# Optimization experiments

Measured on AMD Instinct MI355X. Metric: run time of the kernel, lower is better.

## Reference

```python
import jax, jax.numpy as jnp
import numpy as np

N, E, IN, C, F = 100000, 3200000, 128, 4, 16


def setup_inputs() -> dict:
    key = jax.random.key(0)
    ks = jax.random.split(key, 8)
    return {
        "node_feat": jax.random.normal(ks[0], (N, IN), dtype=jnp.float32),
        "edge_feat": jax.random.normal(ks[1], (E, C), dtype=jnp.float32),
        "src": jax.random.randint(ks[2], (E,), 0, N, dtype=jnp.int32),
        "dst": jax.random.randint(ks[3], (E,), 0, N, dtype=jnp.int32),
        "Wfc": jax.random.normal(ks[4], (C * F, IN), dtype=jnp.float32) * 0.05,
        "We": jax.random.normal(ks[5], (C, C), dtype=jnp.float32) * 0.3,
        "attn_l": jax.random.normal(ks[6], (1, C, F), dtype=jnp.float32) * 0.1,
        "attn_r": jax.random.normal(ks[7], (1, C, F), dtype=jnp.float32) * 0.1,
    }


def reference(node_feat, edge_feat, src, dst, Wfc, We, attn_l, attn_r):
    n = node_feat.shape[0]
    # fc(h).view(-1, C, F)  (shared src/dst projection)
    feat = (node_feat @ Wfc.T).reshape(n, C, F)            # [N, C, F]
    # edge_fc(edge_feat).view(-1, C, 1)
    e_feat = edge_feat @ We.T                               # [E, C]
    # el/er: (feat * attn).sum(-1)
    el = jnp.sum(feat * attn_l, axis=-1)                    # [N, C]
    er = jnp.sum(feat * attn_r, axis=-1)                    # [N, C]
    # u_add_v -> leaky_relu -> * edge feature
    e = jax.nn.leaky_relu(el[src] + er[dst], negative_slope=0.2) * e_feat  # [E, C]
    # edge_softmax grouped by destination node (numerically stable)
    m = jax.ops.segment_max(e, dst, num_segments=n)         # [N, C]
    ee = jnp.exp(e - m[dst])                                # [E, C]
    s = jax.ops.segment_sum(ee, dst, num_segments=n)        # [N, C]
    a = ee / s[dst]                                         # [E, C]
    # message passing: sum_e a_e * ft_src(e)  (standard EGAT aggregation)
    msg = feat[src] * a[:, :, None]                         # [E, C, F]
    rst = jax.ops.segment_sum(msg, dst, num_segments=n)     # [N, C, F]
    return rst
```

## Files before the change

kernel.cpp:

```cpp
#include <hip/hip_runtime.h>
#include <hip/hip_fp16.h>

#define N_NODES 100000
#define N_EDGES 3200000
#define E0 1601536
#define E1REM 1598464
#define BUCKET_NODES 128
#define NB 782
#define NBC 25
#define CNODES 4096
#define CHA 4096
#define NPA0 391
#define NPA1 391
#define CHB 4096
#define NPB0 391
#define NPB1 391
#define FS_CAP 4608
#define NPROJ 782
#define NG64 1563
#define NHIST 512

typedef __attribute__((ext_vector_type(8))) short bf16x8;
typedef __attribute__((ext_vector_type(4))) float f32x4;

__device__ __forceinline__ unsigned short f2bf(float f) {
    unsigned u = __float_as_uint(f);
    unsigned r = (u + 0x7FFFu + ((u >> 16) & 1u)) >> 16;
    return (unsigned short)r;
}
__device__ __forceinline__ float bf2f(unsigned short h) {
    return __uint_as_float(((unsigned)h) << 16);
}

__global__ __launch_bounds__(256) void node_proj(
    const float* __restrict__ node_feat,
    const float* __restrict__ Wfc,
    const float* __restrict__ attn_l,
    const float* __restrict__ attn_r,
    unsigned short* __restrict__ featb,
    float* __restrict__ el,
    float* __restrict__ er)
{
    __shared__ short Wb[8192];
    const int tid = threadIdx.x;
    for (int i = tid; i < 8192; i += 256) {
        const int e   = i & 7;
        const int col = (i >> 3) & 15;
        const int q   = (i >> 7) & 3;
        const int kk  = (i >> 9) & 3;
        const int t   = (i >> 11) & 3;
        Wb[i] = (short)f2bf(Wfc[(t * 16 + col) * 128 + kk * 32 + q * 8 + e]);
    }
    __syncthreads();

    const int lane = tid & 63;
    const int w = tid >> 6;
    const int col = lane & 15;
    const int q = lane >> 4;

    float alv[4], arv[4];
    #pragma unroll
    for (int t = 0; t < 4; ++t) {
        alv[t] = attn_l[t * 16 + col];
        arv[t] = attn_r[t * 16 + col];
    }

    for (int g = blockIdx.x; g < NG64; g += NPROJ) {
        const int n0 = g * 64 + w * 16;
        if (n0 >= N_NODES) continue;

        f32x4 acc0 = {0.f,0.f,0.f,0.f}, acc1 = {0.f,0.f,0.f,0.f};
        f32x4 acc2 = {0.f,0.f,0.f,0.f}, acc3 = {0.f,0.f,0.f,0.f};

        #pragma unroll
        for (int kk = 0; kk < 4; ++kk) {
            const float* ap = node_feat + (size_t)(n0 + col) * 128 + kk * 32 + q * 8;
            const float4 a0 = *(const float4*)ap;
            const float4 a1 = *(const float4*)(ap + 4);
            bf16x8 af;
            af[0] = (short)f2bf(a0.x); af[1] = (short)f2bf(a0.y);
            af[2] = (short)f2bf(a0.z); af[3] = (short)f2bf(a0.w);
            af[4] = (short)f2bf(a1.x); af[5] = (short)f2bf(a1.y);
            af[6] = (short)f2bf(a1.z); af[7] = (short)f2bf(a1.w);

            const bf16x8 b0 = *(const bf16x8*)&Wb[(((0*4+kk)*4+q)*16 + col)*8];
            const bf16x8 b1 = *(const bf16x8*)&Wb[(((1*4+kk)*4+q)*16 + col)*8];
            const bf16x8 b2 = *(const bf16x8*)&Wb[(((2*4+kk)*4+q)*16 + col)*8];
            const bf16x8 b3 = *(const bf16x8*)&Wb[(((3*4+kk)*4+q)*16 + col)*8];
            acc0 = __builtin_amdgcn_mfma_f32_16x16x32_bf16(af, b0, acc0, 0, 0, 0);
            acc1 = __builtin_amdgcn_mfma_f32_16x16x32_bf16(af, b1, acc1, 0, 0, 0);
            acc2 = __builtin_amdgcn_mfma_f32_16x16x32_bf16(af, b2, acc2, 0, 0, 0);
            acc3 = __builtin_amdgcn_mfma_f32_16x16x32_bf16(af, b3, acc3, 0, 0, 0);
        }

        #pragma unroll
        for (int m = 0; m < 4; ++m) {
            const size_t rb = (size_t)(n0 + q * 4 + m) * 64;
            featb[rb + 0 * 16 + col] = f2bf(acc0[m]);
            featb[rb + 1 * 16 + col] = f2bf(acc1[m]);
            featb[rb + 2 * 16 + col] = f2bf(acc2[m]);
            featb[rb + 3 * 16 + col] = f2bf(acc3[m]);
        }

        #pragma unroll
        for (int m = 0; m < 4; ++m) {
            float pl0 = acc0[m] * alv[0], pr0 = acc0[m] * arv[0];
            float pl1 = acc1[m] * alv[1], pr1 = acc1[m] * arv[1];
            float pl2 = acc2[m] * alv[2], pr2 = acc2[m] * arv[2];
            float pl3 = acc3[m] * alv[3], pr3 = acc3[m] * arv[3];
            #pragma unroll
            for (int off = 8; off >= 1; off >>= 1) {
                pl0 += __shfl_xor(pl0, off); pr0 += __shfl_xor(pr0, off);
                pl1 += __shfl_xor(pl1, off); pr1 += __shfl_xor(pr1, off);
                pl2 += __shfl_xor(pl2, off); pr2 += __shfl_xor(pr2, off);
                pl3 += __shfl_xor(pl3, off); pr3 += __shfl_xor(pr3, off);
            }
            if (col == 0) {
                const size_t eb = (size_t)(n0 + q * 4 + m) * 4;
                el[eb + 0] = pl0; el[eb + 1] = pl1; el[eb + 2] = pl2; el[eb + 3] = pl3;
                er[eb + 0] = pr0; er[eb + 1] = pr1; er[eb + 2] = pr2; er[eb + 3] = pr3;
            }
        }
    }
}

__global__ __launch_bounds__(256) void fhist(
    const int* __restrict__ dst,
    int* __restrict__ hhtot)
{
    __shared__ int h[2 * NB];
    const int tid = threadIdx.x;
    for (int i = tid; i < 2 * NB; i += 256) h[i] = 0;
    __syncthreads();
    const int stride = NHIST * 256;
    const int n4 = N_EDGES / 4;
    for (int idx = blockIdx.x * 256 + tid; idx < n4; idx += stride) {
        const int4 d4 = ((const int4*)dst)[idx];
        const int off = (idx * 4 >= E0) ? NB : 0;
        atomicAdd(&h[off + (d4.x >> 7)], 1);
        atomicAdd(&h[off + (d4.y >> 7)], 1);
        atomicAdd(&h[off + (d4.z >> 7)], 1);
        atomicAdd(&h[off + (d4.w >> 7)], 1);
    }
    __syncthreads();
    for (int i = tid; i < 2 * NB; i += 256)
        if (h[i]) atomicAdd(&hhtot[i], h[i]);
}

__global__ __launch_bounds__(64) void bscan(const int* __restrict__ hhtot,
                                            int* __restrict__ base,
                                            int* __restrict__ fcursor,
                                            int* __restrict__ cbaseH,
                                            int* __restrict__ ccursorH)
{
    const int lane = threadIdx.x;
    int carry = 0;
    for (int ch = 0; ch < NB; ch += 64) {
        const int idx = ch + lane;
        const int v = (idx < NB) ? (hhtot[idx] + hhtot[NB + idx]) : 0;
        int x = v;
        #pragma unroll
        for (int off = 1; off < 64; off <<= 1) {
            int y = __shfl_up(x, off);
            if (lane >= off) x += y;
        }
        const int excl = x - v + carry;
        if (idx < NB) { base[idx] = excl; fcursor[idx] = excl; }
        carry += __shfl(x, 63);
    }
    if (lane == 0) base[NB] = carry;

    for (int h2 = 0; h2 < 2; ++h2) {
        int v = 0;
        if (lane < NBC) {
            const int f0 = lane * 32;
            const int f1 = min(f0 + 32, NB);
            for (int f = f0; f < f1; ++f) v += hhtot[h2 * NB + f];
        }
        int x = v;
        #pragma unroll
        for (int off = 1; off < 64; off <<= 1) {
            int y = __shfl_up(x, off);
            if (lane >= off) x += y;
        }
        const int excl = x - v;
        if (lane <= NBC) cbaseH[h2 * (NBC + 1) + lane] = excl;
        if (lane < NBC) ccursorH[h2 * NBC + lane] = excl;
    }
}

__device__ __forceinline__ void passA_body(
    unsigned char* smem,
    const int* __restrict__ src,
    const int* __restrict__ dst,
    const float* __restrict__ edge_feat,
    const float* __restrict__ We,
    const float* __restrict__ el,
    const float* __restrict__ er,
    int* __restrict__ ccursorH,
    uint3* __restrict__ wA,
    int half, int blk)
{
    int* ldst  = (int*)smem;
    int* lbase = (int*)(smem + 16384);
    int* lcnt  = (int*)(smem + 16512);
    const int tid = threadIdx.x;
    if (tid < NBC) lcnt[tid] = 0;
    __syncthreads();
    const int hbeg = half ? E0 : 0;
    const int hend = half ? N_EDGES : E0;
    const int e0 = hbeg + blk * CHA;
    const int n = min(CHA, hend - e0);
    for (int i = tid; i < n; i += 1024) {
        const int d = dst[e0 + i];
        ldst[i] = d;
        atomicAdd(&lcnt[d >> 12], 1);
    }
    __syncthreads();
    if (tid < NBC) {
        const int c = lcnt[tid];
        lbase[tid] = c ? atomicAdd(&ccursorH[half * NBC + tid], c) : 0;
        lcnt[tid] = 0;
    }
    __syncthreads();

    const float4 W0 = ((const float4*)We)[0];
    const float4 W1 = ((const float4*)We)[1];
    const float4 W2 = ((const float4*)We)[2];
    const float4 W3 = ((const float4*)We)[3];

    for (int i = tid; i < n; i += 1024) {
        const int e = e0 + i;
        const int d = ldst[i];
        const int cb = d >> 12;
        const int r = atomicAdd(&lcnt[cb], 1);
        const int pos = lbase[cb] + r;

        const int s = src[e];
        const float4 ef = ((const float4*)edge_feat)[e];
        const float4 l4 = ((const float4*)el)[s];
        const float4 r4 = ((const float4*)er)[d];

        float t0 = l4.x + r4.x; t0 = t0 > 0.f ? t0 : 0.2f * t0;
        float t1 = l4.y + r4.y; t1 = t1 > 0.f ? t1 : 0.2f * t1;
        float t2 = l4.z + r4.z; t2 = t2 > 0.f ? t2 : 0.2f * t2;
        float t3 = l4.w + r4.w; t3 = t3 > 0.f ? t3 : 0.2f * t3;

        const float ee0 = __expf(t0 * (W0.x * ef.x + W0.y * ef.y + W0.z * ef.z + W0.w * ef.w));
        const float ee1 = __expf(t1 * (W1.x * ef.x + W1.y * ef.y + W1.z * ef.z + W1.w * ef.w));
        const float ee2 = __expf(t2 * (W2.x * ef.x + W2.y * ef.y + W2.z * ef.z + W2.w * ef.w));
        const float ee3 = __expf(t3 * (W3.x * ef.x + W3.y * ef.y + W3.z * ef.z + W3.w * ef.w));

        const unsigned h0 = __half_as_ushort(__float2half_rn(ee0));
        const unsigned h1 = __half_as_ushort(__float2half_rn(ee1));
        const unsigned h2 = __half_as_ushort(__float2half_rn(ee2));
        const unsigned h3 = __half_as_ushort(__float2half_rn(ee3));

        wA[pos] = make_uint3((unsigned)s | ((unsigned)(d & (CNODES - 1)) << 17),
                             h0 | (h1 << 16), h2 | (h3 << 16));
    }
}

__device__ __forceinline__ void passB_body(
    unsigned char* smem,
    const int* __restrict__ cbaseH,
    int* __restrict__ fcursor,
    const uint3* __restrict__ wA,
    uint3* __restrict__ wB,
    int half, int blk)
{
    int* lcb   = (int*)smem;
    int* lbase = (int*)(smem + 112);
    int* lcnt  = (int*)(smem + 3240);
    unsigned short* sfid = (unsigned short*)(smem + 6368);
    uint3* sx  = (uint3*)(smem + 14576);
    const int tid = threadIdx.x;
    for (int i = tid; i < NB; i += 1024) lcnt[i] = 0;
    if (tid < NBC + 1) lcb[tid] = cbaseH[half * (NBC + 1) + tid];
    __syncthreads();

    const int hsz = half ? E1REM : E0;
    const int p0 = blk * CHB;
    const int n = min(CHB, hsz - p0);
    for (int i = tid; i < n; i += 1024) {
        const uint3 x = wA[p0 + i];
        sx[i] = x;
        const int pos = p0 + i;
        int lo = 0, hi = NBC;
        while (lo + 1 < hi) {
            const int mid = (lo + hi) >> 1;
            if (lcb[mid] <= pos) lo = mid; else hi = mid;
        }
        const int dst12 = (int)((x.x >> 17) & (CNODES - 1));
        const int fid = lo * 32 + (dst12 >> 7);
        sfid[i] = (unsigned short)fid;
        atomicAdd(&lcnt[fid], 1);
    }
    __syncthreads();
    for (int b = tid; b < NB; b += 1024) {
        const int c = lcnt[b];
        lbase[b] = c ? atomicAdd(&fcursor[b], c) : 0;
        lcnt[b] = 0;
    }
    __syncthreads();
    for (int i = tid; i < n; i += 1024) {
        const uint3 x = sx[i];
        const int fid = sfid[i];
        const int r = atomicAdd(&lcnt[fid], 1);
        const unsigned dl = (x.x >> 17) & (BUCKET_NODES - 1);
        wB[lbase[fid] + r] = make_uint3((x.x & 0x1FFFFu) | (dl << 17), x.y, x.z);
    }
}

__global__ __launch_bounds__(1024) void passA(
    const int* __restrict__ src, const int* __restrict__ dst,
    const float* __restrict__ edge_feat, const float* __restrict__ We,
    const float* __restrict__ el, const float* __restrict__ er,
    int* __restrict__ ccursorH, uint3* __restrict__ wA, int half)
{
    __shared__ __align__(16) unsigned char smem[16640];
    passA_body(smem, src, dst, edge_feat, We, el, er, ccursorH, wA, half, blockIdx.x);
}

__global__ __launch_bounds__(1024) void passB(
    const int* __restrict__ cbaseH, int* __restrict__ fcursor,
    const uint3* __restrict__ wA, uint3* __restrict__ wB, int half)
{
    __shared__ __align__(16) unsigned char smem[63728];
    passB_body(smem, cbaseH, fcursor, wA, wB, half, blockIdx.x);
}

__global__ __launch_bounds__(1024) void finesort(
    const int* __restrict__ base,
    uint3* __restrict__ wP,
    int* __restrict__ node_off)
{
    __shared__ uint3 sP[FS_CAP];
    __shared__ int hist[BUCKET_NODES];
    __shared__ int cur[BUCKET_NODES];
    const int b = blockIdx.x;
    const int s = base[b];
    int cnt = base[b + 1] - s;
    if (cnt > FS_CAP) cnt = FS_CAP;
    const int tid = threadIdx.x;
    if (tid < BUCKET_NODES) hist[tid] = 0;
    __syncthreads();
    for (int i = tid; i < cnt; i += 1024) {
        const uint3 p = wP[s + i];
        sP[i] = p;
        atomicAdd(&hist[(p.x >> 17) & (BUCKET_NODES - 1)], 1);
    }
    __syncthreads();
    if (tid < 64) {
        int carry = 0;
        for (int ch = 0; ch < BUCKET_NODES; ch += 64) {
            const int v = hist[ch + tid];
            int x = v;
            #pragma unroll
            for (int off = 1; off < 64; off <<= 1) {
                int y = __shfl_up(x, off);
                if (tid >= off) x += y;
            }
            const int excl = x - v + carry;
            cur[ch + tid] = excl;
            const int node = b * BUCKET_NODES + ch + tid;
            if (node < N_NODES) node_off[node] = s + excl;
            carry += __shfl(x, 63);
        }
        if (tid == 0 && b == NB - 1) node_off[N_NODES] = N_EDGES;
    }
    __syncthreads();
    for (int i = tid; i < cnt; i += 1024) {
        const uint3 p = sP[i];
        const int dl = (p.x >> 17) & (BUCKET_NODES - 1);
        const int r = atomicAdd(&cur[dl], 1);
        wP[s + r] = make_uint3((p.x & 0x1FFFFu) << 7, p.y, p.z);
    }
}

__global__ __launch_bounds__(256) void aggregate(
    const int* __restrict__ node_off,
    const uint3* __restrict__ wP,
    const unsigned short* __restrict__ featb,
    float* __restrict__ rst)
{
    __shared__ float lee[4][64][4];
    __shared__ unsigned lsi[4][64];
    const int tid = threadIdx.x;
    const int node = (int)((blockIdx.x * 256 + tid) >> 6);
    const int lane = tid & 63;
    const int w = tid >> 6;
    if (node >= N_NODES) return;
    const int half = lane >> 5;
    const int j = lane & 31;
    const int cc = j >> 3;
    const unsigned jByte = (unsigned)j * 4u;
    const unsigned char* __restrict__ fbyte = (const unsigned char*)featb;

    const int start = node_off[node];
    const int end = node_off[node + 1];

    float acc0 = 0.f, acc1 = 0.f;
    float s0 = 0.f, s1 = 0.f, s2 = 0.f, s3 = 0.f;

    for (int bat = start; bat < end; bat += 64) {
        const int n = min(64, end - bat);
        if (lane < n) {
            const uint3 p = wP[bat + lane];
            const float e0 = __half2float(__ushort_as_half((unsigned short)(p.y & 0xffffu)));
            const float e1 = __half2float(__ushort_as_half((unsigned short)(p.y >> 16)));
            const float e2 = __half2float(__ushort_as_half((unsigned short)(p.z & 0xffffu)));
            const float e3 = __half2float(__ushort_as_half((unsigned short)(p.z >> 16)));
            lsi[w][lane] = p.x;
            *(float4*)&lee[w][lane][0] = make_float4(e0, e1, e2, e3);
            s0 += e0; s1 += e1; s2 += e2; s3 += e3;
        } else {
            lsi[w][lane] = 0;
            *(float4*)&lee[w][lane][0] = make_float4(0.f, 0.f, 0.f, 0.f);
        }
        __builtin_amdgcn_wave_barrier();
        const int iters = (n + 1) >> 1;
        for (int i = 0; i < iters; ++i) {
            const int e = 2 * i + half;
            const unsigned so = lsi[w][e];
            const float eec = lee[w][e][cc];
            const unsigned fr = *(const unsigned*)(fbyte + so + jByte);
            acc0 = fmaf(eec, bf2f((unsigned short)(fr & 0xffffu)), acc0);
            acc1 = fmaf(eec, bf2f((unsigned short)(fr >> 16)), acc1);
        }
        __builtin_amdgcn_wave_barrier();
    }

    acc0 += __shfl_xor(acc0, 32);
    acc1 += __shfl_xor(acc1, 32);

    #pragma unroll
    for (int off = 32; off >= 1; off >>= 1) {
        s0 += __shfl_xor(s0, off);
        s1 += __shfl_xor(s1, off);
        s2 += __shfl_xor(s2, off);
        s3 += __shfl_xor(s3, off);
    }

    const float v0 = __shfl(acc0, lane >> 1);
    const float v1 = __shfl(acc1, lane >> 1);
    const float accL = (lane & 1) ? v1 : v0;
    const int c = lane >> 4;
    const float ssum = (c == 0) ? s0 : ((c == 1) ? s1 : ((c == 2) ? s2 : s3));
    rst[(size_t)node * 64 + lane] = (end > start) ? accL / ssum : 0.f;
}

extern "C" void kernel_launch(void* const* d_in, const int* in_sizes, int n_in,
                              void* d_out, int out_size, void* d_ws, size_t ws_size,
                              hipStream_t stream)
{
    const float* node_feat = (const float*)d_in[0];
    const float* edge_feat = (const float*)d_in[1];
    const int*   src       = (const int*)d_in[2];
    const int*   dst       = (const int*)d_in[3];
    const float* Wfc       = (const float*)d_in[4];
    const float* We        = (const float*)d_in[5];
    const float* attn_l    = (const float*)d_in[6];
    const float* attn_r    = (const float*)d_in[7];
    float* rst = (float*)d_out;

    char* ws = (char*)d_ws;
    unsigned short* featb = (unsigned short*)(ws);
    float* el       = (float*)(ws + 12800000);
    float* er       = (float*)(ws + 14400000);
    int*   hhtot    = (int*)  (ws + 16000000);
    int*   base     = (int*)  (ws + 16006400);
    int*   fcursor  = (int*)  (ws + 16009600);
    int*   cbaseH   = (int*)  (ws + 16012800);
    int*   ccursorH = (int*)  (ws + 16013056);
    int*   node_off = (int*)  (ws + 16013312);
    uint3* wB       = (uint3*)(ws + 16413952);
    uint3* wA = (uint3*)d_out;

    hipMemsetAsync(hhtot, 0, 2 * NB * sizeof(int), stream);

    node_proj<<<NPROJ, 256, 0, stream>>>(node_feat, Wfc, attn_l, attn_r, featb, el, er);
    fhist<<<NHIST, 256, 0, stream>>>(dst, hhtot);
    bscan<<<1, 64, 0, stream>>>(hhtot, base, fcursor, cbaseH, ccursorH);

    passA<<<NPA0, 1024, 0, stream>>>(src, dst, edge_feat, We, el, er, ccursorH, wA, 0);
    passB<<<NPB0, 1024, 0, stream>>>(cbaseH, fcursor, wA, wB, 0);
    passA<<<NPA1, 1024, 0, stream>>>(src, dst, edge_feat, We, el, er, ccursorH, wA, 1);
    passB<<<NPB1, 1024, 0, stream>>>(cbaseH, fcursor, wA, wB, 1);

    finesort<<<NB, 1024, 0, stream>>>(base, wB, node_off);
    aggregate<<<(N_NODES * 64 + 255) / 256, 256, 0, stream>>>(node_off, wB, featb, rst);
}
```

Baseline: 240.4 us.

## Replace two-level coarse/fine edge partition with single-pass scatter into fine buckets

```diff
diff --git a/kernel.cpp b/kernel.cpp
--- a/kernel.cpp
+++ b/kernel.cpp
@@ -3,18 +3,10 @@
 
 #define N_NODES 100000
 #define N_EDGES 3200000
-#define E0 1601536
-#define E1REM 1598464
 #define BUCKET_NODES 128
 #define NB 782
-#define NBC 25
-#define CNODES 4096
-#define CHA 4096
-#define NPA0 391
-#define NPA1 391
-#define CHB 4096
-#define NPB0 391
-#define NPB1 391
+#define CHS 8192
+#define NSC 391
 #define FS_CAP 4608
 #define NPROJ 782
 #define NG64 1563
@@ -126,38 +118,35 @@
 
 __global__ __launch_bounds__(256) void fhist(
     const int* __restrict__ dst,
-    int* __restrict__ hhtot)
-{
-    __shared__ int h[2 * NB];
-    const int tid = threadIdx.x;
-    for (int i = tid; i < 2 * NB; i += 256) h[i] = 0;
+    int* __restrict__ ftot)
+{
+    __shared__ int h[NB];
+    const int tid = threadIdx.x;
+    for (int i = tid; i < NB; i += 256) h[i] = 0;
     __syncthreads();
     const int stride = NHIST * 256;
     const int n4 = N_EDGES / 4;
     for (int idx = blockIdx.x * 256 + tid; idx < n4; idx += stride) {
         const int4 d4 = ((const int4*)dst)[idx];
-        const int off = (idx * 4 >= E0) ? NB : 0;
-        atomicAdd(&h[off + (d4.x >> 7)], 1);
-        atomicAdd(&h[off + (d4.y >> 7)], 1);
-        atomicAdd(&h[off + (d4.z >> 7)], 1);
-        atomicAdd(&h[off + (d4.w >> 7)], 1);
-    }
-    __syncthreads();
-    for (int i = tid; i < 2 * NB; i += 256)
-        if (h[i]) atomicAdd(&hhtot[i], h[i]);
-}
-
-__global__ __launch_bounds__(64) void bscan(const int* __restrict__ hhtot,
+        atomicAdd(&h[d4.x >> 7], 1);
+        atomicAdd(&h[d4.y >> 7], 1);
+        atomicAdd(&h[d4.z >> 7], 1);
+        atomicAdd(&h[d4.w >> 7], 1);
+    }
+    __syncthreads();
+    for (int i = tid; i < NB; i += 256)
+        if (h[i]) atomicAdd(&ftot[i], h[i]);
+}
+
+__global__ __launch_bounds__(64) void bscan(const int* __restrict__ ftot,
                                             int* __restrict__ base,
-                                            int* __restrict__ fcursor,
-                                            int* __restrict__ cbaseH,
-                                            int* __restrict__ ccursorH)
+                                            int* __restrict__ fcursor)
 {
     const int lane = threadIdx.x;
     int carry = 0;
     for (int ch = 0; ch < NB; ch += 64) {
         const int idx = ch + lane;
-        const int v = (idx < NB) ? (hhtot[idx] + hhtot[NB + idx]) : 0;
+        const int v = (idx < NB) ? ftot[idx] : 0;
         int x = v;
         #pragma unroll
         for (int off = 1; off < 64; off <<= 1) {
@@ -169,58 +158,36 @@
         carry += __shfl(x, 63);
     }
     if (lane == 0) base[NB] = carry;
-
-    for (int h2 = 0; h2 < 2; ++h2) {
-        int v = 0;
-        if (lane < NBC) {
-            const int f0 = lane * 32;
-            const int f1 = min(f0 + 32, NB);
-            for (int f = f0; f < f1; ++f) v += hhtot[h2 * NB + f];
-        }
-        int x = v;
-        #pragma unroll
-        for (int off = 1; off < 64; off <<= 1) {
-            int y = __shfl_up(x, off);
-            if (lane >= off) x += y;
-        }
-        const int excl = x - v;
-        if (lane <= NBC) cbaseH[h2 * (NBC + 1) + lane] = excl;
-        if (lane < NBC) ccursorH[h2 * NBC + lane] = excl;
-    }
-}
-
-__device__ __forceinline__ void passA_body(
-    unsigned char* smem,
+}
+
+__global__ __launch_bounds__(1024) void scatter(
     const int* __restrict__ src,
     const int* __restrict__ dst,
     const float* __restrict__ edge_feat,
     const float* __restrict__ We,
     const float* __restrict__ el,
     const float* __restrict__ er,
-    int* __restrict__ ccursorH,
-    uint3* __restrict__ wA,
-    int half, int blk)
-{
-    int* ldst  = (int*)smem;
-    int* lbase = (int*)(smem + 16384);
-    int* lcnt  = (int*)(smem + 16512);
-    const int tid = threadIdx.x;
-    if (tid < NBC) lcnt[tid] = 0;
-    __syncthreads();
-    const int hbeg = half ? E0 : 0;
-    const int hend = half ? N_EDGES : E0;
-    const int e0 = hbeg + blk * CHA;
-    const int n = min(CHA, hend - e0);
+    int* __restrict__ fcursor,
+    uint3* __restrict__ wB)
+{
+    __shared__ int ldst[CHS];
+    __shared__ int lbase[NB];
+    __shared__ int lcnt[NB];
+    const int tid = threadIdx.x;
+    for (int i = tid; i < NB; i += 1024) lcnt[i] = 0;
+    __syncthreads();
+    const int e0 = blockIdx.x * CHS;
+    const int n = min(CHS, N_EDGES - e0);
     for (int i = tid; i < n; i += 1024) {
         const int d = dst[e0 + i];
         ldst[i] = d;
-        atomicAdd(&lcnt[d >> 12], 1);
-    }
-    __syncthreads();
-    if (tid < NBC) {
-        const int c = lcnt[tid];
-        lbase[tid] = c ? atomicAdd(&ccursorH[half * NBC + tid], c) : 0;
-        lcnt[tid] = 0;
+        atomicAdd(&lcnt[d >> 7], 1);
+    }
+    __syncthreads();
+    for (int b = tid; b < NB; b += 1024) {
+        const int c = lcnt[b];
+        lbase[b] = c ? atomicAdd(&fcursor[b], c) : 0;
+        lcnt[b] = 0;
     }
     __syncthreads();
 
@@ -232,9 +199,9 @@
     for (int i = tid; i < n; i += 1024) {
         const int e = e0 + i;
         const int d = ldst[i];
-        const int cb = d >> 12;
-        const int r = atomicAdd(&lcnt[cb], 1);
-        const int pos = lbase[cb] + r;
+        const int fb = d >> 7;
+        const int r = atomicAdd(&lcnt[fb], 1);
+        const int pos = lbase[fb] + r;
 
         const int s = src[e];
         const float4 ef = ((const float4*)edge_feat)[e];
@@ -256,78 +223,9 @@
         const unsigned h2 = __half_as_ushort(__float2half_rn(ee2));
         const unsigned h3 = __half_as_ushort(__float2half_rn(ee3));
 
-        wA[pos] = make_uint3((unsigned)s | ((unsigned)(d & (CNODES - 1)) << 17),
+        wB[pos] = make_uint3((unsigned)s | ((unsigned)(d & (BUCKET_NODES - 1)) << 17),
                              h0 | (h1 << 16), h2 | (h3 << 16));
     }
-}
-
-__device__ __forceinline__ void passB_body(
-    unsigned char* smem,
-    const int* __restrict__ cbaseH,
-    int* __restrict__ fcursor,
-    const uint3* __restrict__ wA,
-    uint3* __restrict__ wB,
-    int half, int blk)
-{
-    int* lcb   = (int*)smem;
-    int* lbase = (int*)(smem + 112);
-    int* lcnt  = (int*)(smem + 3240);
-    unsigned short* sfid = (unsigned short*)(smem + 6368);
-    uint3* sx  = (uint3*)(smem + 14576);
-    const int tid = threadIdx.x;
-    for (int i = tid; i < NB; i += 1024) lcnt[i] = 0;
-    if (tid < NBC + 1) lcb[tid] = cbaseH[half * (NBC + 1) + tid];
-    __syncthreads();
-
-    const int hsz = half ? E1REM : E0;
-    const int p0 = blk * CHB;
-    const int n = min(CHB, hsz - p0);
-    for (int i = tid; i < n; i += 1024) {
-        const uint3 x = wA[p0 + i];
-        sx[i] = x;
-        const int pos = p0 + i;
-        int lo = 0, hi = NBC;
-        while (lo + 1 < hi) {
-            const int mid = (lo + hi) >> 1;
-            if (lcb[mid] <= pos) lo = mid; else hi = mid;
-        }
-        const int dst12 = (int)((x.x >> 17) & (CNODES - 1));
-        const int fid = lo * 32 + (dst12 >> 7);
-        sfid[i] = (unsigned short)fid;
-        atomicAdd(&lcnt[fid], 1);
-    }
-    __syncthreads();
-    for (int b = tid; b < NB; b += 1024) {
-        const int c = lcnt[b];
-        lbase[b] = c ? atomicAdd(&fcursor[b], c) : 0;
-        lcnt[b] = 0;
-    }
-    __syncthreads();
-    for (int i = tid; i < n; i += 1024) {
-        const uint3 x = sx[i];
-        const int fid = sfid[i];
-        const int r = atomicAdd(&lcnt[fid], 1);
-        const unsigned dl = (x.x >> 17) & (BUCKET_NODES - 1);
-        wB[lbase[fid] + r] = make_uint3((x.x & 0x1FFFFu) | (dl << 17), x.y, x.z);
-    }
-}
-
-__global__ __launch_bounds__(1024) void passA(
-    const int* __restrict__ src, const int* __restrict__ dst,
-    const float* __restrict__ edge_feat, const float* __restrict__ We,
-    const float* __restrict__ el, const float* __restrict__ er,
-    int* __restrict__ ccursorH, uint3* __restrict__ wA, int half)
-{
-    __shared__ __align__(16) unsigned char smem[16640];
-    passA_body(smem, src, dst, edge_feat, We, el, er, ccursorH, wA, half, blockIdx.x);
-}
-
-__global__ __launch_bounds__(1024) void passB(
-    const int* __restrict__ cbaseH, int* __restrict__ fcursor,
-    const uint3* __restrict__ wA, uint3* __restrict__ wB, int half)
-{
-    __shared__ __align__(16) unsigned char smem[63728];
-    passB_body(smem, cbaseH, fcursor, wA, wB, half, blockIdx.x);
 }
 
 __global__ __launch_bounds__(1024) void finesort(
@@ -468,26 +366,18 @@
     unsigned short* featb = (unsigned short*)(ws);
     float* el       = (float*)(ws + 12800000);
     float* er       = (float*)(ws + 14400000);
-    int*   hhtot    = (int*)  (ws + 16000000);
-    int*   base     = (int*)  (ws + 16006400);
-    int*   fcursor  = (int*)  (ws + 16009600);
-    int*   cbaseH   = (int*)  (ws + 16012800);
-    int*   ccursorH = (int*)  (ws + 16013056);
-    int*   node_off = (int*)  (ws + 16013312);
-    uint3* wB       = (uint3*)(ws + 16413952);
-    uint3* wA = (uint3*)d_out;
-
-    hipMemsetAsync(hhtot, 0, 2 * NB * sizeof(int), stream);
+    int*   ftot     = (int*)  (ws + 16000000);
+    int*   base     = (int*)  (ws + 16003200);
+    int*   fcursor  = (int*)  (ws + 16006400);
+    int*   node_off = (int*)  (ws + 16009600);
+    uint3* wB       = (uint3*)(ws + 16409728);
+
+    hipMemsetAsync(ftot, 0, NB * sizeof(int), stream);
 
     node_proj<<<NPROJ, 256, 0, stream>>>(node_feat, Wfc, attn_l, attn_r, featb, el, er);
-    fhist<<<NHIST, 256, 0, stream>>>(dst, hhtot);
-    bscan<<<1, 64, 0, stream>>>(hhtot, base, fcursor, cbaseH, ccursorH);
-
-    passA<<<NPA0, 1024, 0, stream>>>(src, dst, edge_feat, We, el, er, ccursorH, wA, 0);
-    passB<<<NPB0, 1024, 0, stream>>>(cbaseH, fcursor, wA, wB, 0);
-    passA<<<NPA1, 1024, 0, stream>>>(src, dst, edge_feat, We, el, er, ccursorH, wA, 1);
-    passB<<<NPB1, 1024, 0, stream>>>(cbaseH, fcursor, wA, wB, 1);
-
+    fhist<<<NHIST, 256, 0, stream>>>(dst, ftot);
+    bscan<<<1, 64, 0, stream>>>(ftot, base, fcursor);
+    scatter<<<NSC, 1024, 0, stream>>>(src, dst, edge_feat, We, el, er, fcursor, wB);
     finesort<<<NB, 1024, 0, stream>>>(base, wB, node_off);
     aggregate<<<(N_NODES * 64 + 255) / 256, 256, 0, stream>>>(node_off, wB, featb, rst);
 }
```

New measurement: 270.9 us. +12.7%, slower.

## Fuse per-bucket fine sort with aggregation using an LDS permutation index

Applied to the files above, without the earlier changes.

```diff
diff --git a/kernel.cpp b/kernel.cpp
--- a/kernel.cpp
+++ b/kernel.cpp
@@ -330,13 +330,17 @@
     passB_body(smem, cbaseH, fcursor, wA, wB, half, blockIdx.x);
 }
 
-__global__ __launch_bounds__(1024) void finesort(
+__global__ __launch_bounds__(1024) void sort_agg(
     const int* __restrict__ base,
-    uint3* __restrict__ wP,
-    int* __restrict__ node_off)
-{
-    __shared__ uint3 sP[FS_CAP];
+    const uint3* __restrict__ wP,
+    const unsigned short* __restrict__ featb,
+    float* __restrict__ rst)
+{
+    __shared__ unsigned sA[FS_CAP];
+    __shared__ unsigned sE[FS_CAP * 2];
+    __shared__ unsigned short inv[FS_CAP];
     __shared__ int hist[BUCKET_NODES];
+    __shared__ int off[BUCKET_NODES + 1];
     __shared__ int cur[BUCKET_NODES];
     const int b = blockIdx.x;
     const int s = base[b];
@@ -345,109 +349,89 @@
     const int tid = threadIdx.x;
     if (tid < BUCKET_NODES) hist[tid] = 0;
     __syncthreads();
+
     for (int i = tid; i < cnt; i += 1024) {
         const uint3 p = wP[s + i];
-        sP[i] = p;
+        sA[i] = p.x;
+        sE[2 * i]     = p.y;
+        sE[2 * i + 1] = p.z;
         atomicAdd(&hist[(p.x >> 17) & (BUCKET_NODES - 1)], 1);
     }
     __syncthreads();
+
     if (tid < 64) {
         int carry = 0;
         for (int ch = 0; ch < BUCKET_NODES; ch += 64) {
             const int v = hist[ch + tid];
             int x = v;
             #pragma unroll
-            for (int off = 1; off < 64; off <<= 1) {
-                int y = __shfl_up(x, off);
-                if (tid >= off) x += y;
+            for (int o = 1; o < 64; o <<= 1) {
+                int y = __shfl_up(x, o);
+                if (tid >= o) x += y;
             }
             const int excl = x - v + carry;
+            off[ch + tid] = excl;
             cur[ch + tid] = excl;
-            const int node = b * BUCKET_NODES + ch + tid;
-            if (node < N_NODES) node_off[node] = s + excl;
             carry += __shfl(x, 63);
         }
-        if (tid == 0 && b == NB - 1) node_off[N_NODES] = N_EDGES;
-    }
-    __syncthreads();
+        if (tid == 0) off[BUCKET_NODES] = carry;
+    }
+    __syncthreads();
+
     for (int i = tid; i < cnt; i += 1024) {
-        const uint3 p = sP[i];
-        const int dl = (p.x >> 17) & (BUCKET_NODES - 1);
+        const unsigned a = sA[i];
+        const int dl = (int)((a >> 17) & (BUCKET_NODES - 1));
         const int r = atomicAdd(&cur[dl], 1);
-        wP[s + r] = make_uint3((p.x & 0x1FFFFu) << 7, p.y, p.z);
-    }
-}
-
-__global__ __launch_bounds__(256) void aggregate(
-    const int* __restrict__ node_off,
-    const uint3* __restrict__ wP,
-    const unsigned short* __restrict__ featb,
-    float* __restrict__ rst)
-{
-    __shared__ float lee[4][64][4];
-    __shared__ unsigned lsi[4][64];
-    const int tid = threadIdx.x;
-    const int node = (int)((blockIdx.x * 256 + tid) >> 6);
+        inv[r] = (unsigned short)i;
+        sA[i] = (a & 0x1FFFFu) << 7;
+    }
+    __syncthreads();
+
     const int lane = tid & 63;
     const int w = tid >> 6;
-    if (node >= N_NODES) return;
     const int half = lane >> 5;
     const int j = lane & 31;
     const int cc = j >> 3;
     const unsigned jByte = (unsigned)j * 4u;
     const unsigned char* __restrict__ fbyte = (const unsigned char*)featb;
-
-    const int start = node_off[node];
-    const int end = node_off[node + 1];
-
-    float acc0 = 0.f, acc1 = 0.f;
-    float s0 = 0.f, s1 = 0.f, s2 = 0.f, s3 = 0.f;
-
-    for (int bat = start; bat < end; bat += 64) {
-        const int n = min(64, end - bat);
-        if (lane < n) {
-            const uint3 p = wP[bat + lane];
-            const float e0 = __half2float(__ushort_as_half((unsigned short)(p.y & 0xffffu)));
-            const float e1 = __half2float(__ushort_as_half((unsigned short)(p.y >> 16)));
-            const float e2 = __half2float(__ushort_as_half((unsigned short)(p.z & 0xffffu)));
-            const float e3 = __half2float(__ushort_as_half((unsigned short)(p.z >> 16)));
-            lsi[w][lane] = p.x;
-            *(float4*)&lee[w][lane][0] = make_float4(e0, e1, e2, e3);
-            s0 += e0; s1 += e1; s2 += e2; s3 += e3;
-        } else {
-            lsi[w][lane] = 0;
-            *(float4*)&lee[w][lane][0] = make_float4(0.f, 0.f, 0.f, 0.f);
-        }
-        __builtin_amdgcn_wave_barrier();
-        const int iters = (n + 1) >> 1;
+    const int node0 = b * BUCKET_NODES;
+
+    #pragma unroll 1
+    for (int nn = 0; nn < 8; ++nn) {
+        const int nl = w * 8 + nn;
+        const int node = node0 + nl;
+        if (node >= N_NODES) break;
+        const int st = off[nl];
+        const int deg = off[nl + 1] - st;
+
+        float acc0 = 0.f, acc1 = 0.f, scc = 0.f;
+        const int iters = (deg + 1) >> 1;
         for (int i = 0; i < iters; ++i) {
-            const int e = 2 * i + half;
-            const unsigned so = lsi[w][e];
-            const float eec = lee[w][e][cc];
+            const int o = 2 * i + half;
+            const bool valid = o < deg;
+            const int pos = valid ? (st + o) : 0;
+            const int idx = (int)inv[pos];
+            const unsigned so = sA[idx];
+            const unsigned ed = sE[2 * idx + (cc >> 1)];
+            float eec = __half2float(__ushort_as_half(
+                (unsigned short)((cc & 1) ? (ed >> 16) : (ed & 0xffffu))));
+            if (!valid) eec = 0.f;
             const unsigned fr = *(const unsigned*)(fbyte + so + jByte);
             acc0 = fmaf(eec, bf2f((unsigned short)(fr & 0xffffu)), acc0);
             acc1 = fmaf(eec, bf2f((unsigned short)(fr >> 16)), acc1);
-        }
-        __builtin_amdgcn_wave_barrier();
-    }
-
-    acc0 += __shfl_xor(acc0, 32);
-    acc1 += __shfl_xor(acc1, 32);
-
-    #pragma unroll
-    for (int off = 32; off >= 1; off >>= 1) {
-        s0 += __shfl_xor(s0, off);
-        s1 += __shfl_xor(s1, off);
-        s2 += __shfl_xor(s2, off);
-        s3 += __shfl_xor(s3, off);
-    }
-
-    const float v0 = __shfl(acc0, lane >> 1);
-    const float v1 = __shfl(acc1, lane >> 1);
-    const float accL = (lane & 1) ? v1 : v0;
-    const int c = lane >> 4;
-    const float ssum = (c == 0) ? s0 : ((c == 1) ? s1 : ((c == 2) ? s2 : s3));
-    rst[(size_t)node * 64 + lane] = (end > start) ? accL / ssum : 0.f;
+            scc += eec;
+        }
+
+        const float a0 = acc0 + __shfl_xor(acc0, 32);
+        const float a1 = acc1 + __shfl_xor(acc1, 32);
+        const float ss = scc + __shfl_xor(scc, 32);
+
+        const float v0 = __shfl(a0, lane >> 1);
+        const float v1 = __shfl(a1, lane >> 1);
+        const float sv = __shfl(ss, lane >> 1);
+        const float accL = (lane & 1) ? v1 : v0;
+        rst[(size_t)node * 64 + lane] = (deg > 0) ? accL / sv : 0.f;
+    }
 }
 
 extern "C" void kernel_launch(void* const* d_in, const int* in_sizes, int n_in,
@@ -473,8 +457,7 @@
     int*   fcursor  = (int*)  (ws + 16009600);
     int*   cbaseH   = (int*)  (ws + 16012800);
     int*   ccursorH = (int*)  (ws + 16013056);
-    int*   node_off = (int*)  (ws + 16013312);
-    uint3* wB       = (uint3*)(ws + 16413952);
+    uint3* wB       = (uint3*)(ws + 16013312);
     uint3* wA = (uint3*)d_out;
 
     hipMemsetAsync(hhtot, 0, 2 * NB * sizeof(int), stream);
@@ -488,6 +471,5 @@
     passA<<<NPA1, 1024, 0, stream>>>(src, dst, edge_feat, We, el, er, ccursorH, wA, 1);
     passB<<<NPB1, 1024, 0, stream>>>(cbaseH, fcursor, wA, wB, 1);
 
-    finesort<<<NB, 1024, 0, stream>>>(base, wB, node_off);
-    aggregate<<<(N_NODES * 64 + 255) / 256, 256, 0, stream>>>(node_off, wB, featb, rst);
-}
+    sort_agg<<<NB, 1024, 0, stream>>>(base, wB, featb, rst);
+}
```

Measured after the change: 231.3 us. 1.04x faster.
